# Kernel tuning notes

Hardware: AMD Instinct MI355X
Metric: run time of the kernel (lower is better)

The kernel has to match this reference:

```python
import jax, jax.numpy as jnp
import numpy as np

SIZE = 896
HALF = SIZE // 2
BINS = 256  # 2 ** (16 / 2)


def _scale(idx):
    # map bin index [0, BINS-1] -> [-1, 1]
    return idx.astype(jnp.float32) / ((BINS - 1) / 2.0) - 1.0


def setup_inputs() -> dict:
    key = jax.random.key(0)
    ks = jax.random.split(key, 13)
    B, T = 32, 256
    rn = lambda k, shape, s: jax.random.normal(k, shape, dtype=jnp.float32) * s
    return {
        "conditional": rn(ks[0], (B, T, 3, SIZE), 0.1),
        "hidden_state": rn(ks[1], (B, SIZE), 0.1),
        "gru_input_bias": rn(ks[2], (3 * SIZE,), 0.1),
        "gru_hidden_weight": rn(ks[3], (3 * SIZE, SIZE), 0.05),
        "gru_hidden_bias": rn(ks[4], (3 * SIZE,), 0.1),
        "w_coarse_in": rn(ks[5], (3 * HALF, 2), 0.5),
        "b_coarse_in": rn(ks[6], (3 * HALF,), 0.1),
        "w_fine_in": rn(ks[7], (3 * HALF, 3), 0.5),
        "b_fine_in": rn(ks[8], (3 * HALF,), 0.1),
        "w_bins_coarse": rn(ks[9], (BINS, HALF), 0.05),
        "b_bins_coarse": rn(ks[10], (BINS,), 0.1),
        "w_bins_fine": rn(ks[11], (BINS, HALF), 0.05),
        "b_bins_fine": rn(ks[12], (BINS,), 0.1),
    }


def reference(conditional, hidden_state, gru_input_bias, gru_hidden_weight,
              gru_hidden_bias, w_coarse_in, b_coarse_in, w_fine_in, b_fine_in,
              w_bins_coarse, b_bins_coarse, w_bins_fine, b_bins_fine):
    B = conditional.shape[0]
    # add GRU input biases per gate (r, u, e)
    cond = conditional + gru_input_bias.reshape(3, SIZE)  # [B,T,3,SIZE]
    # split each gate into coarse/fine halves and regroup: [B,T,3*HALF]
    cond_c = jnp.concatenate([cond[:, :, 0, :HALF], cond[:, :, 1, :HALF], cond[:, :, 2, :HALF]], axis=-1)
    cond_f = jnp.concatenate([cond[:, :, 0, HALF:], cond[:, :, 1, HALF:], cond[:, :, 2, HALF:]], axis=-1)
    cond_c = jnp.swapaxes(cond_c, 0, 1)  # [T,B,3*HALF] time-major for scan
    cond_f = jnp.swapaxes(cond_f, 0, 1)

    # initial go-sample: split_signal(0) -> coarse bin 128, fine bin 0
    coarse0 = jnp.full((B, 1), 128.0 / 127.5 - 1.0, dtype=jnp.float32)
    fine0 = jnp.full((B, 1), -1.0, dtype=jnp.float32)
    ch0 = hidden_state[:, :HALF]
    fh0 = hidden_state[:, HALF:]

    def step(carry, x):
        coarse, fine, ch, fh = carry
        xc, xf = x
        hp = jnp.concatenate([ch, fh], axis=1) @ gru_hidden_weight.T + gru_hidden_bias  # [B,3*SIZE]
        hcr, hfr, hcu, hfu, hce, hfe = jnp.split(hp, 6, axis=1)  # each [B,HALF]
        # ---- coarse half-GRU ----
        ci = jnp.concatenate([coarse, fine], axis=1)  # [B,2]
        cp = ci @ w_coarse_in.T + b_coarse_in + xc  # [B,3*HALF]
        ru = jax.nn.sigmoid(cp[:, :SIZE] + jnp.concatenate([hcr, hcu], axis=1))
        r, u = ru[:, :HALF], ru[:, HALF:]
        e = jnp.tanh(r * hce + cp[:, SIZE:])
        ch = u * ch + (1.0 - u) * e
        c_idx = jnp.argmax(ch @ w_bins_coarse.T + b_bins_coarse, axis=1)  # [B]
        coarse = _scale(c_idx)[:, None]
        # ---- fine half-GRU ----
        fi = jnp.concatenate([ci, coarse], axis=1)  # [B,3]
        fp = fi @ w_fine_in.T + b_fine_in + xf
        ru = jax.nn.sigmoid(fp[:, :SIZE] + jnp.concatenate([hfr, hfu], axis=1))
        r, u = ru[:, :HALF], ru[:, HALF:]
        e = jnp.tanh(r * hfe + fp[:, SIZE:])
        fh = u * fh + (1.0 - u) * e
        f_idx = jnp.argmax(fh @ w_bins_fine.T + b_bins_fine, axis=1)
        fine = _scale(f_idx)[:, None]
        return (coarse, fine, ch, fh), (c_idx, f_idx)

    (_, _, ch, fh), (oc, of) = jax.lax.scan(step, (coarse0, fine0, ch0, fh0), (cond_c, cond_f))
    hidden = jnp.concatenate([ch, fh], axis=1)  # [B,SIZE]
    return jnp.swapaxes(oc, 0, 1), jnp.swapaxes(of, 0, 1), hidden
```

## Files before the change

kernel.cpp:

```cpp
#include <hip/hip_runtime.h>

#define NWG  56
#define NBLK 57
#define NTHR 384
#define TT   256
#define SPLITF   2048.0f
#define INVSPLIT 4.8828125e-4f

typedef _Float16 f16;
typedef __attribute__((ext_vector_type(8))) _Float16 f16x8;
typedef __attribute__((ext_vector_type(4))) float f32x4;

__device__ __forceinline__ float sigacc(float x){ return 1.0f/(1.0f + expf(-x)); }

__device__ __forceinline__ unsigned long long amax_key(float v, int bin, unsigned tag){
  unsigned u = __float_as_uint(v);
  u = (u & 0x80000000u) ? ~u : (u | 0x80000000u);
  return ((unsigned long long)u << 32) | ((unsigned long long)(tag & 0xFFFFu) << 8)
       | (unsigned)(255 - bin);
}

__device__ __forceinline__ int grp_base(int g){ return 448 * ((g < 3) ? (2*g) : (2*g - 5)); }

__device__ __forceinline__ void xchg32(unsigned* p, unsigned v){
  __hip_atomic_exchange(p, v, __ATOMIC_RELAXED, __HIP_MEMORY_SCOPE_AGENT);
}
__device__ __forceinline__ void xchg64(unsigned long long* p, unsigned long long v){
  __hip_atomic_exchange(p, v, __ATOMIC_RELAXED, __HIP_MEMORY_SCOPE_AGENT);
}
__device__ __forceinline__ unsigned ldg32(const unsigned* p){
  return __hip_atomic_load(p, __ATOMIC_RELAXED, __HIP_MEMORY_SCOPE_AGENT);
}
__device__ __forceinline__ unsigned long long ldg64(const void* p){
  return __hip_atomic_load((const unsigned long long*)p, __ATOMIC_RELAXED, __HIP_MEMORY_SCOPE_AGENT);
}
__device__ __forceinline__ void drain(){ asm volatile("s_waitcnt vmcnt(0)" ::: "memory"); }
__device__ __forceinline__ int f16bits(f16 h){
  return (int)__builtin_bit_cast(unsigned short, h);
}

__global__ void pack_gru(const float* __restrict__ W, f16* __restrict__ outH, f16* __restrict__ outL){
  int blk = blockIdx.x;
  int ks  = blk % 14;
  int rest= blk / 14;
  int wv  = rest % 6, w = rest / 6;
  int mt  = wv >> 1, kh = wv & 1;
  int l   = threadIdx.x;
  int lr  = mt*16 + (l & 15);
  int R   = grp_base(lr >> 3) + 8*w + (lr & 7);
  int k   = kh*448 + ks*32 + (l >> 4)*8;
  const float* src = W + (size_t)R*896 + k;
  f16x8 vh, vl;
  #pragma unroll
  for (int i=0;i<8;i++){
    float x = src[i];
    f16 h = (f16)x;
    vh[i] = h;
    vl[i] = (f16)((x - (float)h) * SPLITF);
  }
  size_t o = (size_t)blk*64 + l;
  ((f16x8*)outH)[o] = vh;
  ((f16x8*)outL)[o] = vl;
}

__global__ void pack_bins(const float* __restrict__ Wc, const float* __restrict__ Wf,
                          f16* __restrict__ oCh, f16* __restrict__ oCl,
                          f16* __restrict__ oFh, f16* __restrict__ oFl){
  int blk  = blockIdx.x;
  int half = blk / 224;
  int rem  = blk % 224;
  int ks   = rem % 14, wg = rem / 14;
  int l    = threadIdx.x;
  const float* W = half ? Wf : Wc;
  f16* oh = half ? oFh : oCh;
  f16* ol = half ? oFl : oCl;
  int bin = wg*16 + (l & 15);
  int k   = ks*32 + (l >> 4)*8;
  const float* src = W + (size_t)bin*448 + k;
  f16x8 vh, vl;
  #pragma unroll
  for (int i=0;i<8;i++){
    float x = src[i];
    f16 h = (f16)x;
    vh[i] = h;
    vl[i] = (f16)((x - (float)h) * SPLITF);
  }
  size_t o = (size_t)rem*64 + l;
  ((f16x8*)oh)[o] = vh;
  ((f16x8*)ol)[o] = vl;
}

__launch_bounds__(NTHR, 1)
__global__ void wavernn_main(
    const float* __restrict__ cond,
    const float* __restrict__ h0,
    const float* __restrict__ gib,
    const float* __restrict__ ghb,
    const float* __restrict__ wci,
    const float* __restrict__ bci,
    const float* __restrict__ wfi,
    const float* __restrict__ bfi,
    const float* __restrict__ bbc,
    const float* __restrict__ bbf,
    const f16*  __restrict__ wsAh, const f16* __restrict__ wsAl,
    const f16*  __restrict__ wsBCh, const f16* __restrict__ wsBCl,
    const f16*  __restrict__ wsBFh, const f16* __restrict__ wsBFl,
    unsigned*   __restrict__ Hg,
    unsigned long long* __restrict__ partC,
    unsigned long long* __restrict__ partF,
    unsigned*   __restrict__ flags,
    unsigned*   __restrict__ resC,
    unsigned*   __restrict__ resF,
    float* __restrict__ out)
{
  __shared__ float hpL[48][33];
  __shared__ float coarseL[32], fineL[32];
  __shared__ f16x8 binBh0[896], binBl0[896], binBh1[896], binBl1[896];
  __shared__ float wclL[3][8][2], bclL[3][8], wflL[3][8][3], bflL[3][8], hblL[48];

  const int w   = blockIdx.x;
  const int tid = threadIdx.x;
  const int wv  = tid >> 6;
  const int l   = tid & 63;

  auto poll_parts = [&](const unsigned long long* part, unsigned tgt)->unsigned long long {
    int bb = l & 31;
    unsigned long long k0,k1,k2,k3,k4,k5,k6,k7,k8,k9,k10,k11,k12,k13,k14,k15;
    for(;;){
      k0=ldg64(&part[0*32+bb]);  k1=ldg64(&part[1*32+bb]);
      k2=ldg64(&part[2*32+bb]);  k3=ldg64(&part[3*32+bb]);
      k4=ldg64(&part[4*32+bb]);  k5=ldg64(&part[5*32+bb]);
      k6=ldg64(&part[6*32+bb]);  k7=ldg64(&part[7*32+bb]);
      k8=ldg64(&part[8*32+bb]);  k9=ldg64(&part[9*32+bb]);
      k10=ldg64(&part[10*32+bb]); k11=ldg64(&part[11*32+bb]);
      k12=ldg64(&part[12*32+bb]); k13=ldg64(&part[13*32+bb]);
      k14=ldg64(&part[14*32+bb]); k15=ldg64(&part[15*32+bb]);
      unsigned long long tmask = 0xFFFF00ull, texp = (unsigned long long)tgt << 8;
      bool ok = ((k0&tmask)==texp) & ((k1&tmask)==texp) & ((k2&tmask)==texp) & ((k3&tmask)==texp)
              & ((k4&tmask)==texp) & ((k5&tmask)==texp) & ((k6&tmask)==texp) & ((k7&tmask)==texp)
              & ((k8&tmask)==texp) & ((k9&tmask)==texp) & ((k10&tmask)==texp)& ((k11&tmask)==texp)
              & ((k12&tmask)==texp)& ((k13&tmask)==texp)& ((k14&tmask)==texp)& ((k15&tmask)==texp);
      if (__all(ok)) break;
      __builtin_amdgcn_s_sleep(1);
    }
    unsigned long long m01=k0>k1?k0:k1, m23=k2>k3?k2:k3, m45=k4>k5?k4:k5, m67=k6>k7?k6:k7;
    unsigned long long m89=k8>k9?k8:k9, mab=k10>k11?k10:k11, mcd=k12>k13?k12:k13, mef=k14>k15?k14:k15;
    unsigned long long a=m01>m23?m01:m23, c2=m45>m67?m45:m67, d=m89>mab?m89:mab, f=mcd>mef?mcd:mef;
    unsigned long long x=a>c2?a:c2, y=d>f?d:f;
    return x>y?x:y;
  };

  if (w == NWG) {
    if (wv == 0) {
      for (int t=0; t<TT; t++){
        unsigned tgt = (unsigned)(t+1);
        unsigned long long best = poll_parts(partC, tgt);
        int bin = 255 - (int)(best & 0xFFull);
        if (l < 32) {
          out[l*TT + t] = (float)bin;
          xchg32(&resC[l*16], (tgt << 16) | (unsigned)bin);
        }
      }
    } else if (wv == 1) {
      for (int t=0; t<TT; t++){
        unsigned tgt = (unsigned)(t+1);
        unsigned long long best = poll_parts(partF, tgt);
        int bin = 255 - (int)(best & 0xFFull);
        if (l < 32) {
          out[8192 + l*TT + t] = (float)bin;
          xchg32(&resF[l*16], (tgt << 16) | (unsigned)bin);
        }
      }
    }
    return;
  }

  const int b   = tid >> 3, e = tid & 7;
  const bool owner = tid < 256;
  const int jc  = 8*w + e;

  unsigned* fE0 = flags;
  unsigned* fE1 = flags + 1024;
  unsigned* fE3 = flags + 2048;

  const int g_kh = (wv >= 2 && wv <= 4) ? 0 : 1;
  const int g_mt = (wv >= 2 && wv <= 4) ? (wv - 2) : (wv == 5 ? 2 : wv);

  f16x8 afh[14], afl[14];
  {
    const f16x8* Ah = (const f16x8*)wsAh + (size_t)(w*6 + (g_mt*2 + g_kh))*14*64;
    const f16x8* Al = (const f16x8*)wsAl + (size_t)(w*6 + (g_mt*2 + g_kh))*14*64;
    #pragma unroll
    for (int ks=0; ks<14; ks++){ afh[ks] = Ah[ks*64 + l]; afl[ks] = Al[ks*64 + l]; }
  }
  if (w < 16) {
    const f16x8* s0 = (const f16x8*)wsBCh + (size_t)w*896;
    const f16x8* s1 = (const f16x8*)wsBCl + (size_t)w*896;
    const f16x8* s2 = (const f16x8*)wsBFh + (size_t)w*896;
    const f16x8* s3 = (const f16x8*)wsBFl + (size_t)w*896;
    for (int i = tid; i < 896; i += NTHR) {
      binBh0[i] = s0[i]; binBl0[i] = s1[i];
      binBh1[i] = s2[i]; binBl1[i] = s3[i];
    }
  }
  if (tid < 48) hblL[tid] = ghb[grp_base(tid>>3) + 8*w + (tid&7)];
  if (tid < 24) {
    int p = tid >> 3, ee = tid & 7;
    int j = p*448 + 8*w + ee;
    wclL[p][ee][0] = wci[j*2+0]; wclL[p][ee][1] = wci[j*2+1];
    bclL[p][ee]    = bci[j] + gib[p*896 + 8*w + ee];
    wflL[p][ee][0] = wfi[j*3+0]; wflL[p][ee][1] = wfi[j*3+1]; wflL[p][ee][2] = wfi[j*3+2];
    bflL[p][ee]    = bfi[j] + gib[p*896 + 448 + 8*w + ee];
  }
  if (tid < 32) { coarseL[tid] = 128.0f/127.5f - 1.0f; fineL[tid] = -1.0f; }
  float biasC = 0.f, biasF = 0.f;
  if (w < 16) { biasC = bbc[w*16 + (l&15)]; biasF = bbf[w*16 + (l&15)]; }

  auto store_half = [&](unsigned* Hc, int fine, float val){
    f16 hh = (f16)val;
    f16 hl = (f16)((val - (float)hh) * SPLITF);
    int pk = f16bits(hh) | (f16bits(hl) << 16);
    int n1 = __shfl_down(pk, 1);
    int n2 = __shfl_down(pk, 2);
    int n3 = __shfl_down(pk, 3);
    if ((e & 3) == 0) {
      unsigned h0_ = (unsigned)((pk & 0xffff) | (n1 << 16));
      unsigned h1_ = (unsigned)((n2 & 0xffff) | (n3 << 16));
      unsigned l0_ = ((unsigned)pk >> 16) | ((unsigned)n1 & 0xffff0000u);
      unsigned l1_ = ((unsigned)n2 >> 16) | ((unsigned)n3 & 0xffff0000u);
      int q = e >> 2;
      xchg64((unsigned long long*)(Hc + fine*8 + q*2),
             (unsigned long long)h0_ | ((unsigned long long)h1_ << 32));
      xchg64((unsigned long long*)(Hc + fine*8 + 4 + q*2),
             (unsigned long long)l0_ | ((unsigned long long)l1_ << 32));
    }
  };

  auto wait56 = [&](const unsigned* f, int n, unsigned tgt){
    const unsigned* p = f + ((l < n) ? l*16 : 0);
    for(;;){
      unsigned v = ldg32(p);
      if (__all(v == tgt)) break;
      __builtin_amdgcn_s_sleep(1);
    }
    unsigned vv = __hip_atomic_load(p, __ATOMIC_ACQUIRE, __HIP_MEMORY_SCOPE_AGENT);
    asm volatile("" :: "v"(vv) : "memory");
  };
  auto poll_res = [&](const unsigned* res, unsigned tgt)->int{
    const unsigned* p = res + (l & 31)*16;
    unsigned v;
    for(;;){
      v = ldg32(p);
      if (__all((v >> 16) == tgt)) break;
      __builtin_amdgcn_s_sleep(1);
    }
    asm volatile("" ::: "memory");
    return (int)(v & 0xFFFFu);
  };

  float chS = 0.f, fhS = 0.f;
  if (owner) {
    chS = h0[b*896 + jc];
    fhS = h0[b*896 + 448 + jc];
    unsigned* Hc = Hg + (b*56 + w)*16;
    store_half(Hc, 0, chS);
    store_half(Hc, 1, fhS);
  }
  drain();
  __syncthreads();
  if (tid == 0) xchg32(&fE0[w*16], 1u);
  if (wv == 0) wait56(fE0, 56, 1u);
  __syncthreads();

  float xcr=0, xcu=0, xce=0, xfr=0, xfu=0, xfe=0;
  auto prefetch = [&](int t){
    if (owner) {
      const float* cb_ = cond + ((size_t)b*TT + t)*2688;
      xcr = cb_[jc];        xcu = cb_[896 + jc];  xce = cb_[1792 + jc];
      xfr = cb_[448 + jc];  xfu = cb_[1344 + jc]; xfe = cb_[2240 + jc];
    }
  };
  auto gemm_half = [&](const unsigned* H, bool add){
    f32x4 ah0={0,0,0,0}, al0={0,0,0,0}, ah1={0,0,0,0}, al1={0,0,0,0};
    const unsigned* c0 = H + ((size_t)(l&15)*56 + (l>>4))*16 + g_kh*8;
    const unsigned* c1 = c0 + 16*56*16;
    #pragma unroll
    for (int ks=0; ks<14; ks++) {
      const unsigned* p0 = c0 + ks*64;
      const unsigned* p1 = c1 + ks*64;
      f16x8 bh0 = *(const f16x8*)(p0);
      f16x8 bl0 = *(const f16x8*)(p0 + 4);
      f16x8 bh1 = *(const f16x8*)(p1);
      f16x8 bl1 = *(const f16x8*)(p1 + 4);
      ah0 = __builtin_amdgcn_mfma_f32_16x16x32_f16(afh[ks], bh0, ah0, 0,0,0);
      al0 = __builtin_amdgcn_mfma_f32_16x16x32_f16(afh[ks], bl0, al0, 0,0,0);
      al0 = __builtin_amdgcn_mfma_f32_16x16x32_f16(afl[ks], bh0, al0, 0,0,0);
      ah1 = __builtin_amdgcn_mfma_f32_16x16x32_f16(afh[ks], bh1, ah1, 0,0,0);
      al1 = __builtin_amdgcn_mfma_f32_16x16x32_f16(afh[ks], bl1, al1, 0,0,0);
      al1 = __builtin_amdgcn_mfma_f32_16x16x32_f16(afl[ks], bh1, al1, 0,0,0);
    }
    #pragma unroll
    for (int i=0;i<4;i++){
      int row = g_mt*16 + (l>>4)*4 + i;
      float v0 = ah0[i] + al0[i]*INVSPLIT;
      float v1 = ah1[i] + al1[i]*INVSPLIT;
      if (!add) {
        hpL[row][l&15]      = v0 + hblL[row];
        hpL[row][16+(l&15)] = v1 + hblL[row];
      } else {
        hpL[row][l&15]      += v0;
        hpL[row][16+(l&15)] += v1;
      }
    }
  };
  auto do_bins = [&](const unsigned* H, int fine, const f16x8* Bh, const f16x8* Bl,
                     float bias, unsigned long long* part, unsigned tgt, int ntb){
    f32x4 acch={0,0,0,0}, accl={0,0,0,0};
    const unsigned* ar = H + ((size_t)(ntb*16 + (l&15))*56 + (l>>4))*16 + fine*8;
    #pragma unroll
    for (int ks=0; ks<14; ks++) {
      const unsigned* p = ar + ks*64;
      f16x8 ah  = *(const f16x8*)(p);
      f16x8 al_ = *(const f16x8*)(p + 4);
      f16x8 bh = Bh[ks*64 + l];
      f16x8 bl = Bl[ks*64 + l];
      acch = __builtin_amdgcn_mfma_f32_16x16x32_f16(ah,  bh, acch, 0,0,0);
      accl = __builtin_amdgcn_mfma_f32_16x16x32_f16(ah,  bl, accl, 0,0,0);
      accl = __builtin_amdgcn_mfma_f32_16x16x32_f16(al_, bh, accl, 0,0,0);
    }
    #pragma unroll
    for (int i=0;i<4;i++){
      unsigned long long key = amax_key(acch[i] + accl[i]*INVSPLIT + bias, w*16 + (l&15), tgt);
      #pragma unroll
      for (int m=1; m<16; m<<=1){
        unsigned long long o = __shfl_xor(key, m, 16);
        key = (o > key) ? o : key;
      }
      if ((l&15)==0) xchg64(&part[w*32 + ntb*16 + (l>>4)*4 + i], key);
    }
  };

  prefetch(0);
  if (g_kh == 0) gemm_half(Hg, false);
  __syncthreads();
  if (g_kh == 1) gemm_half(Hg, true);
  __syncthreads();

  for (int t=0; t<TT; t++) {
    unsigned* Hn = Hg + (((t+1)&1) ? 28672 : 0);
    const unsigned tgt = (unsigned)(t+1);

    float cprev = 0.f, fprev = 0.f, hfr_ = 0.f, hfu_ = 0.f, hfe_ = 0.f;
    if (owner) {
      cprev = coarseL[b]; fprev = fineL[b];
      float cpr = cprev*wclL[0][e][0] + fprev*wclL[0][e][1] + bclL[0][e] + xcr;
      float cpu_= cprev*wclL[1][e][0] + fprev*wclL[1][e][1] + bclL[1][e] + xcu;
      float cpe = cprev*wclL[2][e][0] + fprev*wclL[2][e][1] + bclL[2][e] + xce;
      float r  = sigacc(cpr  + hpL[e][b]);
      float u  = sigacc(cpu_ + hpL[8+e][b]);
      float g  = tanhf(fmaf(r, hpL[16+e][b], cpe));
      hfr_ = hpL[24+e][b]; hfu_ = hpL[32+e][b]; hfe_ = hpL[40+e][b];
      chS = fmaf(u, chS - g, g);
      store_half(Hn + (b*56 + w)*16, 0, chS);
    }
    drain();
    __syncthreads();
    if (tid == 0) xchg32(&fE1[w*16], tgt);
    if (wv == 0) wait56(fE1, 56, tgt);
    __syncthreads();

    if (w < 16 && wv < 2) do_bins(Hn, 0, binBh0, binBl0, biasC, partC, tgt, wv);
    if (g_kh == 0) gemm_half(Hn, false);
    if (wv == 5) {
      int bin = poll_res(resC, tgt);
      if (l < 32) coarseL[l] = (float)bin * (1.0f/127.5f) - 1.0f;
    }
    __syncthreads();

    if (owner) {
      float cnew = coarseL[b];
      float fpr = cprev*wflL[0][e][0] + fprev*wflL[0][e][1] + cnew*wflL[0][e][2] + bflL[0][e] + xfr;
      float fpu = cprev*wflL[1][e][0] + fprev*wflL[1][e][1] + cnew*wflL[1][e][2] + bflL[1][e] + xfu;
      float fpe = cprev*wflL[2][e][0] + fprev*wflL[2][e][1] + cnew*wflL[2][e][2] + bflL[2][e] + xfe;
      float r  = sigacc(fpr + hfr_);
      float u  = sigacc(fpu + hfu_);
      float g  = tanhf(fmaf(r, hfe_, fpe));
      fhS = fmaf(u, fhS - g, g);
      store_half(Hn + (b*56 + w)*16, 1, fhS);
    }
    drain();
    __syncthreads();
    if (tid == 0) xchg32(&fE3[w*16], tgt);
    if (t < TT-1) prefetch(t+1);
    if (wv == 0) wait56(fE3, 56, tgt);
    __syncthreads();

    if (w < 16 && (wv == 2 || wv == 3)) do_bins(Hn, 1, binBh1, binBl1, biasF, partF, tgt, wv-2);
    if (g_kh == 1) gemm_half(Hn, true);
    if (wv == 4) {
      int bin = poll_res(resF, tgt);
      if (l < 32) fineL[l] = (float)bin * (1.0f/127.5f) - 1.0f;
    }
    __syncthreads();
  }

  if (owner) {
    out[16384 + b*896 + jc]        = chS;
    out[16384 + b*896 + 448 + jc]  = fhS;
  }
}

#define WS_AH    0u
#define WS_AL    4816896u
#define WS_BCH   9633792u
#define WS_BCL   9863168u
#define WS_BFH   10092544u
#define WS_BFL   10321920u
#define WS_HG    10551296u
#define WS_FLAGS 10780672u
#define WS_RES   10792960u
#define WS_PC    10797056u
#define WS_PF    10801152u

extern "C" void kernel_launch(void* const* d_in, const int* in_sizes, int n_in,
                              void* d_out, int out_size, void* d_ws, size_t ws_size,
                              hipStream_t stream) {
  const float* conditional = (const float*)d_in[0];
  const float* hidden0     = (const float*)d_in[1];
  const float* gib         = (const float*)d_in[2];
  const float* ghw         = (const float*)d_in[3];
  const float* ghb         = (const float*)d_in[4];
  const float* wci         = (const float*)d_in[5];
  const float* bci         = (const float*)d_in[6];
  const float* wfi         = (const float*)d_in[7];
  const float* bfi         = (const float*)d_in[8];
  const float* wbc         = (const float*)d_in[9];
  const float* bbc         = (const float*)d_in[10];
  const float* wbf         = (const float*)d_in[11];
  const float* bbf         = (const float*)d_in[12];

  char* ws = (char*)d_ws;
  f16* wsAh  = (f16*)(ws + WS_AH);
  f16* wsAl  = (f16*)(ws + WS_AL);
  f16* wsBCh = (f16*)(ws + WS_BCH);
  f16* wsBCl = (f16*)(ws + WS_BCL);
  f16* wsBFh = (f16*)(ws + WS_BFH);
  f16* wsBFl = (f16*)(ws + WS_BFL);
  unsigned* Hg = (unsigned*)(ws + WS_HG);
  unsigned* flags = (unsigned*)(ws + WS_FLAGS);
  unsigned* resC = (unsigned*)(ws + WS_RES);
  unsigned* resF = (unsigned*)(ws + WS_RES + 2048);
  unsigned long long* partC = (unsigned long long*)(ws + WS_PC);
  unsigned long long* partF = (unsigned long long*)(ws + WS_PF);
  float* out = (float*)d_out;

  hipMemsetAsync(ws + WS_FLAGS, 0, 24576, stream);
  pack_gru<<<dim3(56*6*14), dim3(64), 0, stream>>>(ghw, wsAh, wsAl);
  pack_bins<<<dim3(448), dim3(64), 0, stream>>>(wbc, wbf, wsBCh, wsBCl, wsBFh, wsBFl);
  wavernn_main<<<dim3(NBLK), dim3(NTHR), 0, stream>>>(
      conditional, hidden0, gib, ghb, wci, bci, wfi, bfi, bbc, bbf,
      wsAh, wsAl, wsBCh, wsBCl, wsBFh, wsBFl,
      Hg, partC, partF, flags, resC, resF, out);
}
```

Baseline: 5.578 ms.

## Remove dedicated argmax-reducer block; each workgroup reduces bin partials itself

Drops the extra 57th workgroup that polled the 16 argmax partials and republished the winning bin through a result array. Each of the 56 workers now polls the partials directly with one wave, reducing 8 keys per half-wave and combining the halves with a cross-lane shuffle. Workgroup 0 writes the output indices. This removes one global publish/poll hop per coarse and fine step from the serial critical path. In exchange every workgroup polls the partial buffers, which adds memory traffic to those lines.

```diff
diff --git a/kernel.cpp b/kernel.cpp
--- a/kernel.cpp
+++ b/kernel.cpp
@@ -1,7 +1,6 @@
 #include <hip/hip_runtime.h>
 
 #define NWG  56
-#define NBLK 57
 #define NTHR 384
 #define TT   256
 #define SPLITF   2048.0f
@@ -109,8 +108,6 @@
     unsigned long long* __restrict__ partC,
     unsigned long long* __restrict__ partF,
     unsigned*   __restrict__ flags,
-    unsigned*   __restrict__ resC,
-    unsigned*   __restrict__ resF,
     float* __restrict__ out)
 {
   __shared__ float hpL[48][33];
@@ -122,59 +119,6 @@
   const int tid = threadIdx.x;
   const int wv  = tid >> 6;
   const int l   = tid & 63;
-
-  auto poll_parts = [&](const unsigned long long* part, unsigned tgt)->unsigned long long {
-    int bb = l & 31;
-    unsigned long long k0,k1,k2,k3,k4,k5,k6,k7,k8,k9,k10,k11,k12,k13,k14,k15;
-    for(;;){
-      k0=ldg64(&part[0*32+bb]);  k1=ldg64(&part[1*32+bb]);
-      k2=ldg64(&part[2*32+bb]);  k3=ldg64(&part[3*32+bb]);
-      k4=ldg64(&part[4*32+bb]);  k5=ldg64(&part[5*32+bb]);
-      k6=ldg64(&part[6*32+bb]);  k7=ldg64(&part[7*32+bb]);
-      k8=ldg64(&part[8*32+bb]);  k9=ldg64(&part[9*32+bb]);
-      k10=ldg64(&part[10*32+bb]); k11=ldg64(&part[11*32+bb]);
-      k12=ldg64(&part[12*32+bb]); k13=ldg64(&part[13*32+bb]);
-      k14=ldg64(&part[14*32+bb]); k15=ldg64(&part[15*32+bb]);
-      unsigned long long tmask = 0xFFFF00ull, texp = (unsigned long long)tgt << 8;
-      bool ok = ((k0&tmask)==texp) & ((k1&tmask)==texp) & ((k2&tmask)==texp) & ((k3&tmask)==texp)
-              & ((k4&tmask)==texp) & ((k5&tmask)==texp) & ((k6&tmask)==texp) & ((k7&tmask)==texp)
-              & ((k8&tmask)==texp) & ((k9&tmask)==texp) & ((k10&tmask)==texp)& ((k11&tmask)==texp)
-              & ((k12&tmask)==texp)& ((k13&tmask)==texp)& ((k14&tmask)==texp)& ((k15&tmask)==texp);
-      if (__all(ok)) break;
-      __builtin_amdgcn_s_sleep(1);
-    }
-    unsigned long long m01=k0>k1?k0:k1, m23=k2>k3?k2:k3, m45=k4>k5?k4:k5, m67=k6>k7?k6:k7;
-    unsigned long long m89=k8>k9?k8:k9, mab=k10>k11?k10:k11, mcd=k12>k13?k12:k13, mef=k14>k15?k14:k15;
-    unsigned long long a=m01>m23?m01:m23, c2=m45>m67?m45:m67, d=m89>mab?m89:mab, f=mcd>mef?mcd:mef;
-    unsigned long long x=a>c2?a:c2, y=d>f?d:f;
-    return x>y?x:y;
-  };
-
-  if (w == NWG) {
-    if (wv == 0) {
-      for (int t=0; t<TT; t++){
-        unsigned tgt = (unsigned)(t+1);
-        unsigned long long best = poll_parts(partC, tgt);
-        int bin = 255 - (int)(best & 0xFFull);
-        if (l < 32) {
-          out[l*TT + t] = (float)bin;
-          xchg32(&resC[l*16], (tgt << 16) | (unsigned)bin);
-        }
-      }
-    } else if (wv == 1) {
-      for (int t=0; t<TT; t++){
-        unsigned tgt = (unsigned)(t+1);
-        unsigned long long best = poll_parts(partF, tgt);
-        int bin = 255 - (int)(best & 0xFFull);
-        if (l < 32) {
-          out[8192 + l*TT + t] = (float)bin;
-          xchg32(&resF[l*16], (tgt << 16) | (unsigned)bin);
-        }
-      }
-    }
-    return;
-  }
-
   const int b   = tid >> 3, e = tid & 7;
   const bool owner = tid < 256;
   const int jc  = 8*w + e;
@@ -246,16 +190,26 @@
     unsigned vv = __hip_atomic_load(p, __ATOMIC_ACQUIRE, __HIP_MEMORY_SCOPE_AGENT);
     asm volatile("" :: "v"(vv) : "memory");
   };
-  auto poll_res = [&](const unsigned* res, unsigned tgt)->int{
-    const unsigned* p = res + (l & 31)*16;
-    unsigned v;
+  auto poll16 = [&](const unsigned long long* part, unsigned tgt)->int{
+    int bb = l & 31, off = (l >> 5)*8;
+    unsigned long long k0,k1,k2,k3,k4,k5,k6,k7;
     for(;;){
-      v = ldg32(p);
-      if (__all((v >> 16) == tgt)) break;
+      k0=ldg64(&part[(off+0)*32+bb]); k1=ldg64(&part[(off+1)*32+bb]);
+      k2=ldg64(&part[(off+2)*32+bb]); k3=ldg64(&part[(off+3)*32+bb]);
+      k4=ldg64(&part[(off+4)*32+bb]); k5=ldg64(&part[(off+5)*32+bb]);
+      k6=ldg64(&part[(off+6)*32+bb]); k7=ldg64(&part[(off+7)*32+bb]);
+      unsigned long long tmask = 0xFFFF00ull, texp = (unsigned long long)tgt << 8;
+      bool ok = ((k0&tmask)==texp) & ((k1&tmask)==texp) & ((k2&tmask)==texp) & ((k3&tmask)==texp)
+              & ((k4&tmask)==texp) & ((k5&tmask)==texp) & ((k6&tmask)==texp) & ((k7&tmask)==texp);
+      if (__all(ok)) break;
       __builtin_amdgcn_s_sleep(1);
     }
-    asm volatile("" ::: "memory");
-    return (int)(v & 0xFFFFu);
+    unsigned long long m01=k0>k1?k0:k1, m23=k2>k3?k2:k3, m45=k4>k5?k4:k5, m67=k6>k7?k6:k7;
+    unsigned long long a=m01>m23?m01:m23, c2=m45>m67?m45:m67;
+    unsigned long long best = a>c2?a:c2;
+    unsigned long long o = __shfl_xor(best, 32);
+    best = (o > best) ? o : best;
+    return 255 - (int)(best & 0xFFull);
   };
 
   float chS = 0.f, fhS = 0.f;
@@ -372,8 +326,11 @@
     if (w < 16 && wv < 2) do_bins(Hn, 0, binBh0, binBl0, biasC, partC, tgt, wv);
     if (g_kh == 0) gemm_half(Hn, false);
     if (wv == 5) {
-      int bin = poll_res(resC, tgt);
-      if (l < 32) coarseL[l] = (float)bin * (1.0f/127.5f) - 1.0f;
+      int bin = poll16(partC, tgt);
+      if (l < 32) {
+        coarseL[l] = (float)bin * (1.0f/127.5f) - 1.0f;
+        if (w == 0) out[l*TT + t] = (float)bin;
+      }
     }
     __syncthreads();
 
@@ -398,8 +355,11 @@
     if (w < 16 && (wv == 2 || wv == 3)) do_bins(Hn, 1, binBh1, binBl1, biasF, partF, tgt, wv-2);
     if (g_kh == 1) gemm_half(Hn, true);
     if (wv == 4) {
-      int bin = poll_res(resF, tgt);
-      if (l < 32) fineL[l] = (float)bin * (1.0f/127.5f) - 1.0f;
+      int bin = poll16(partF, tgt);
+      if (l < 32) {
+        fineL[l] = (float)bin * (1.0f/127.5f) - 1.0f;
+        if (w == 0) out[8192 + l*TT + t] = (float)bin;
+      }
     }
     __syncthreads();
   }
@@ -418,9 +378,8 @@
 #define WS_BFL   10321920u
 #define WS_HG    10551296u
 #define WS_FLAGS 10780672u
-#define WS_RES   10792960u
-#define WS_PC    10797056u
-#define WS_PF    10801152u
+#define WS_PC    10793984u
+#define WS_PF    10798080u
 
 extern "C" void kernel_launch(void* const* d_in, const int* in_sizes, int n_in,
                               void* d_out, int out_size, void* d_ws, size_t ws_size,
@@ -448,17 +407,15 @@
   f16* wsBFl = (f16*)(ws + WS_BFL);
   unsigned* Hg = (unsigned*)(ws + WS_HG);
   unsigned* flags = (unsigned*)(ws + WS_FLAGS);
-  unsigned* resC = (unsigned*)(ws + WS_RES);
-  unsigned* resF = (unsigned*)(ws + WS_RES + 2048);
   unsigned long long* partC = (unsigned long long*)(ws + WS_PC);
   unsigned long long* partF = (unsigned long long*)(ws + WS_PF);
   float* out = (float*)d_out;
 
-  hipMemsetAsync(ws + WS_FLAGS, 0, 24576, stream);
+  hipMemsetAsync(ws + WS_FLAGS, 0, 21504, stream);
   pack_gru<<<dim3(56*6*14), dim3(64), 0, stream>>>(ghw, wsAh, wsAl);
   pack_bins<<<dim3(448), dim3(64), 0, stream>>>(wbc, wbf, wsBCh, wsBCl, wsBFh, wsBFl);
-  wavernn_main<<<dim3(NBLK), dim3(NTHR), 0, stream>>>(
+  wavernn_main<<<dim3(NWG), dim3(NTHR), 0, stream>>>(
       conditional, hidden0, gib, ghb, wci, bci, wfi, bfi, bbc, bbf,
       wsAh, wsAl, wsBCh, wsBCl, wsBFh, wsBFl,
-      Hg, partC, partF, flags, resC, resF, out);
-}
+      Hg, partC, partF, flags, out);
+}
```

Result: slower. 5.781 ms (+3.6%).
